# Kernel optimization log

Measured on AMD Instinct MI355X. Metric: run time of the kernel, lower is better.

The kernel has to match this reference:

```python
import jax, jax.numpy as jnp
import numpy as np

WINDOW = 3
SEQ_LEN = 41
FEATURE = 128
FILTER_NUM = 128
PAD = WINDOW // 2


def setup_inputs() -> dict:
    key = jax.random.key(0)
    k1, k2 = jax.random.split(key)
    B = 4096
    inputs = jax.random.normal(k1, (B, SEQ_LEN, FEATURE), dtype=jnp.float32)
    # per-position Linear weights: 41 independent [window*feature -> filter_num] layers
    fan_in = WINDOW * FEATURE
    W = jax.random.normal(k2, (SEQ_LEN, fan_in, FILTER_NUM), dtype=jnp.float32) / np.sqrt(fan_in)
    b = jnp.zeros((SEQ_LEN, FILTER_NUM), dtype=jnp.float32)
    return {"inputs": inputs, "W": W, "b": b}


def reference(inputs, W, b):
    # inputs: [B, S, F]; pad sequence dim by PAD zeros on each side
    xpad = jnp.pad(inputs, ((0, 0), (PAD, PAD), (0, 0)))  # [B, S+2*PAD, F]
    # gather windows: idx[s, w] = s + w -> [B, S, WINDOW, F]
    idx = jnp.arange(SEQ_LEN)[:, None] + jnp.arange(WINDOW)[None, :]
    xw = xpad[:, idx, :]
    B = inputs.shape[0]
    xw = xw.reshape(B, SEQ_LEN, WINDOW * FEATURE)  # [B, S, W*F]
    # per-position linear (locally-connected): one batched GEMM over positions
    out = jnp.einsum('bsd,sdf->bsf', xw, W) + b[None, :, :]
    # ReLU; Dropout(0.5) is identity in eval mode
    return jax.nn.relu(out)
```

## Files before the change

### kernel.cpp

```cpp
#include <hip/hip_runtime.h>

#define SEQ 41
#define FEAT 128
#define KDIM 384
#define ROWLEN (SEQ * FEAT)
#define BM 128

typedef float floatx4 __attribute__((ext_vector_type(4)));
typedef __bf16 bf16x8 __attribute__((ext_vector_type(8)));
typedef unsigned short ushortx4 __attribute__((ext_vector_type(4)));
typedef unsigned short ushortx8 __attribute__((ext_vector_type(8)));

__device__ __forceinline__ unsigned short f2bf(float f) {
    unsigned int u = __builtin_bit_cast(unsigned int, f);
    return (unsigned short)((u + 0x7fffu + ((u >> 16) & 1u)) >> 16);
}

#define DMA16(g, l)                                                          \
    __builtin_amdgcn_global_load_lds(                                        \
        (const __attribute__((address_space(1))) void*)(g),                  \
        (__attribute__((address_space(3))) void*)(l), 16, 0, 0)

__global__ __launch_bounds__(256) void wt2_kernel(const float* __restrict__ W,
                                                  unsigned short* __restrict__ Wt2) {
    int t = blockIdx.x * 256 + threadIdx.x;
    int s = t / 6144, g = t % 6144;
    int lane = g & 63, nt = (g >> 6) & 7, ks = (g >> 9) & 1, slab = g >> 10;
    int n  = nt * 16 + (lane & 15);
    int k0 = slab * 64 + ks * 32 + (lane >> 4) * 8;
    const float* Ws = W + (size_t)s * KDIM * FEAT;
    ushortx8 v;
#pragma unroll
    for (int j = 0; j < 8; j++) v[j] = f2bf(Ws[(size_t)(k0 + j) * FEAT + n]);
    *reinterpret_cast<ushortx8*>(Wt2 + (size_t)t * 8) = v;
}

template <int USE_WT>
__global__ __launch_bounds__(256, 2) void gemm_kernel(const float* __restrict__ X,
                                                      const void* __restrict__ Wsrc,
                                                      const float* __restrict__ bias,
                                                      float* __restrict__ out) {
    __shared__ unsigned short Afrag[2][2][8][512];
    __shared__ unsigned short Bfrag[2][2][8][512];

    const int tid  = threadIdx.x;
    const int lane = tid & 63;
    const int wv   = tid >> 6;
    const int s    = blockIdx.y;
    const int m0   = blockIdx.x * BM;

    const int klo = (s == 0) ? 2 : 0;
    const int khi = (s == SEQ - 1) ? 4 : 6;
    const int nk  = khi - klo;
    const int obase = (s - 1) * FEAT;

    const int colq = lane & 15, quad = lane >> 4;
    const int wr = wv >> 1, wc = wv & 1;

    const int ar = tid >> 3;
    const int ag = tid & 7;
    const int aq = ag >> 1, ahalf = ag & 1;

    const unsigned short* Wt2 = (const unsigned short*)Wsrc;
    const float* Wf = (const float*)Wsrc;

    floatx4 acc[4][4];
#pragma unroll
    for (int i = 0; i < 4; i++)
#pragma unroll
        for (int j = 0; j < 4; j++) acc[i][j] = (floatx4){0.f, 0.f, 0.f, 0.f};

    floatx4 a0[4], a1[4];

    auto stageA_load = [&](int kki) {
#pragma unroll
        for (int p = 0; p < 4; p++) {
            const float* base = X + (size_t)(m0 + p * 32 + ar) * ROWLEN
                                  + obase + kki * 64 + ag * 4;
            a0[p] = *reinterpret_cast<const floatx4*>(base);
            a1[p] = *reinterpret_cast<const floatx4*>(base + 32);
        }
    };
    auto stageA_write = [&](int buf) {
#pragma unroll
        for (int p = 0; p < 4; p++) {
            int r  = p * 32 + ar;
            int mt = r >> 4;
            int sl = ((r & 15) + 16 * aq) * 8 + ahalf * 4;
            ushortx4 w0, w1;
#pragma unroll
            for (int e = 0; e < 4; e++) { w0[e] = f2bf(a0[p][e]); w1[e] = f2bf(a1[p][e]); }
            *reinterpret_cast<ushortx4*>(&Afrag[buf][0][mt][sl]) = w0;
            *reinterpret_cast<ushortx4*>(&Afrag[buf][1][mt][sl]) = w1;
        }
    };
    auto stageB = [&](int buf, int kki) {
        if (USE_WT) {
            const unsigned short* src = Wt2 + (size_t)(s * 6 + kki) * 8192;
#pragma unroll
            for (int j = 0; j < 4; j++) {
                int fid = wv * 4 + j;
                const unsigned short* g = src + fid * 512 + lane * 8;
                DMA16(g, &Bfrag[buf][fid >> 3][fid & 7][0]);
            }
        } else {
#pragma unroll
            for (int p = 0; p < 4; p++) {
                int g2 = p * 256 + tid;
                int ln = g2 & 63, nt = (g2 >> 6) & 7, ks = (g2 >> 9) & 1;
                int n = nt * 16 + (ln & 15);
                int k = kki * 64 + ks * 32 + (ln >> 4) * 8;
                ushortx8 v;
#pragma unroll
                for (int j = 0; j < 8; j++)
                    v[j] = f2bf(Wf[((size_t)s * KDIM + k + j) * FEAT + n]);
                *reinterpret_cast<ushortx8*>(&Bfrag[buf][ks][nt][ln * 8]) = v;
            }
        }
    };
    auto compute = [&](int buf) {
#pragma unroll
        for (int ks = 0; ks < 2; ks++) {
            bf16x8 af[4], bf[4];
#pragma unroll
            for (int i = 0; i < 4; i++)
                af[i] = *reinterpret_cast<const bf16x8*>(&Afrag[buf][ks][wr * 4 + i][lane * 8]);
#pragma unroll
            for (int i = 0; i < 4; i++)
                bf[i] = *reinterpret_cast<const bf16x8*>(&Bfrag[buf][ks][wc * 4 + i][lane * 8]);
#pragma unroll
            for (int mi = 0; mi < 4; mi++)
#pragma unroll
                for (int ni = 0; ni < 4; ni++)
                    acc[mi][ni] = __builtin_amdgcn_mfma_f32_16x16x32_bf16(
                        af[mi], bf[ni], acc[mi][ni], 0, 0, 0);
        }
    };

    stageA_load(klo);
    stageB(0, klo);
    stageA_write(0);

    for (int i = 0; i < nk; i++) {
        __syncthreads();
        int cur = i & 1, nxt = cur ^ 1;
        if (i + 1 < nk) {
            stageA_load(klo + i + 1);
            stageB(nxt, klo + i + 1);
        }
        compute(cur);
        if (i + 1 < nk) stageA_write(nxt);
    }

#pragma unroll
    for (int mi = 0; mi < 4; mi++) {
        int m = m0 + (wr * 4 + mi) * 16 + quad * 4;
#pragma unroll
        for (int ni = 0; ni < 4; ni++) {
            int n = (wc * 4 + ni) * 16 + colq;
            float bv = bias[s * FEAT + n];
#pragma unroll
            for (int r = 0; r < 4; r++) {
                float v = acc[mi][ni][r] + bv;
                v = v > 0.f ? v : 0.f;
                out[((size_t)(m + r) * SEQ + s) * FEAT + n] = v;
            }
        }
    }
}

extern "C" void kernel_launch(void* const* d_in, const int* in_sizes, int n_in,
                              void* d_out, int out_size, void* d_ws, size_t ws_size,
                              hipStream_t stream) {
    const float* X    = (const float*)d_in[0];
    const float* W    = (const float*)d_in[1];
    const float* bias = (const float*)d_in[2];
    float* out = (float*)d_out;

    const int B = in_sizes[0] / ROWLEN;
    dim3 grid(B / BM, SEQ);

    const size_t wt_bytes = (size_t)SEQ * 6 * 8192 * sizeof(unsigned short);
    if (ws_size >= wt_bytes) {
        unsigned short* Wt2 = (unsigned short*)d_ws;
        wt2_kernel<<<(SEQ * 6144) / 256, 256, 0, stream>>>(W, Wt2);
        gemm_kernel<1><<<grid, 256, 0, stream>>>(X, (const void*)Wt2, bias, out);
    } else {
        gemm_kernel<0><<<grid, 256, 0, stream>>>(X, (const void*)W, bias, out);
    }
}
```

Before: 184.2 us.

## Load B fragments directly to registers, tile-transpose weights, raise occupancy

The weight pre-transpose kernel now stages each 64x128 slab through shared memory so both the fp32 reads and the bf16 writes are coalesced. It also uses the hardware bf16 conversion. The GEMM drops the shared-memory B buffer and its LDS DMA: each wave loads its own B fragments straight from global memory into registers, one slab at a time. The K loop is fully unrolled over 6 slabs, with zero-filled A at the boundary positions. Launch bounds rise to 3 blocks per CU. Freeing LDS and the B writes should allow more blocks per CU, at the cost of B loads that are not prefetched and extra MFMA work on zero padding for the edge positions.

Measured after the change: 232.2 us. +26.1%, slower.

```diff
diff --git a/kernel.cpp b/kernel.cpp
--- a/kernel.cpp
+++ b/kernel.cpp
@@ -12,56 +12,59 @@
 typedef unsigned short ushortx8 __attribute__((ext_vector_type(8)));
 
 __device__ __forceinline__ unsigned short f2bf(float f) {
-    unsigned int u = __builtin_bit_cast(unsigned int, f);
-    return (unsigned short)((u + 0x7fffu + ((u >> 16) & 1u)) >> 16);
+    return __builtin_bit_cast(unsigned short, (__bf16)f);
 }
 
-#define DMA16(g, l)                                                          \
-    __builtin_amdgcn_global_load_lds(                                        \
-        (const __attribute__((address_space(1))) void*)(g),                  \
-        (__attribute__((address_space(3))) void*)(l), 16, 0, 0)
-
-__global__ __launch_bounds__(256) void wt2_kernel(const float* __restrict__ W,
-                                                  unsigned short* __restrict__ Wt2) {
-    int t = blockIdx.x * 256 + threadIdx.x;
-    int s = t / 6144, g = t % 6144;
-    int lane = g & 63, nt = (g >> 6) & 7, ks = (g >> 9) & 1, slab = g >> 10;
-    int n  = nt * 16 + (lane & 15);
-    int k0 = slab * 64 + ks * 32 + (lane >> 4) * 8;
-    const float* Ws = W + (size_t)s * KDIM * FEAT;
-    ushortx8 v;
+__global__ __launch_bounds__(256) void wt3_kernel(const float* __restrict__ W,
+                                                  unsigned short* __restrict__ Wt) {
+    __shared__ float tile[64][FEAT + 1];
+    const int tid = threadIdx.x;
+    const int s = blockIdx.x / 6, slab = blockIdx.x % 6;
+    const float* src = W + ((size_t)s * KDIM + slab * 64) * FEAT;
 #pragma unroll
-    for (int j = 0; j < 8; j++) v[j] = f2bf(Ws[(size_t)(k0 + j) * FEAT + n]);
-    *reinterpret_cast<ushortx8*>(Wt2 + (size_t)t * 8) = v;
+    for (int p = 0; p < 8; p++) {
+        int q  = p * 256 + tid;
+        int k  = q >> 5;
+        int n4 = (q & 31) * 4;
+        floatx4 v = *reinterpret_cast<const floatx4*>(src + (size_t)k * FEAT + n4);
+        tile[k][n4] = v[0]; tile[k][n4 + 1] = v[1];
+        tile[k][n4 + 2] = v[2]; tile[k][n4 + 3] = v[3];
+    }
+    __syncthreads();
+    unsigned short* dst = Wt + (size_t)blockIdx.x * 8192;
+#pragma unroll
+    for (int p = 0; p < 4; p++) {
+        int g = p * 256 + tid;
+        int lane = g & 63, nt = (g >> 6) & 7, ks = g >> 9;
+        int n  = nt * 16 + (lane & 15);
+        int k0 = ks * 32 + (lane >> 4) * 8;
+        ushortx8 v;
+#pragma unroll
+        for (int j = 0; j < 8; j++) v[j] = f2bf(tile[k0 + j][n]);
+        *reinterpret_cast<ushortx8*>(dst + (size_t)g * 8) = v;
+    }
 }
 
 template <int USE_WT>
-__global__ __launch_bounds__(256, 2) void gemm_kernel(const float* __restrict__ X,
+__global__ __launch_bounds__(256, 3) void gemm_kernel(const float* __restrict__ X,
                                                       const void* __restrict__ Wsrc,
                                                       const float* __restrict__ bias,
                                                       float* __restrict__ out) {
     __shared__ unsigned short Afrag[2][2][8][512];
-    __shared__ unsigned short Bfrag[2][2][8][512];
 
     const int tid  = threadIdx.x;
     const int lane = tid & 63;
     const int wv   = tid >> 6;
     const int s    = blockIdx.y;
     const int m0   = blockIdx.x * BM;
-
-    const int klo = (s == 0) ? 2 : 0;
-    const int khi = (s == SEQ - 1) ? 4 : 6;
-    const int nk  = khi - klo;
     const int obase = (s - 1) * FEAT;
 
+    const int wr = wv >> 1, wc = wv & 1;
     const int colq = lane & 15, quad = lane >> 4;
-    const int wr = wv >> 1, wc = wv & 1;
-
-    const int ar = tid >> 3;
-    const int ag = tid & 7;
+    const int ar = tid >> 3, ag = tid & 7;
     const int aq = ag >> 1, ahalf = ag & 1;
 
-    const unsigned short* Wt2 = (const unsigned short*)Wsrc;
+    const unsigned short* Wt = (const unsigned short*)Wsrc;
     const float* Wf = (const float*)Wsrc;
 
     floatx4 acc[4][4];
@@ -71,14 +74,24 @@
         for (int j = 0; j < 4; j++) acc[i][j] = (floatx4){0.f, 0.f, 0.f, 0.f};
 
     floatx4 a0[4], a1[4];
+    bf16x8 bq[2][4];
 
-    auto stageA_load = [&](int kki) {
+    auto stageA_load = [&](int slab) {
+        bool valid = !((s == 0 && slab < 2) || (s == SEQ - 1 && slab >= 4));
+        if (valid) {
 #pragma unroll
-        for (int p = 0; p < 4; p++) {
-            const float* base = X + (size_t)(m0 + p * 32 + ar) * ROWLEN
-                                  + obase + kki * 64 + ag * 4;
-            a0[p] = *reinterpret_cast<const floatx4*>(base);
-            a1[p] = *reinterpret_cast<const floatx4*>(base + 32);
+            for (int p = 0; p < 4; p++) {
+                const float* base = X + (size_t)(m0 + p * 32 + ar) * ROWLEN
+                                      + obase + slab * 64 + ag * 4;
+                a0[p] = *reinterpret_cast<const floatx4*>(base);
+                a1[p] = *reinterpret_cast<const floatx4*>(base + 32);
+            }
+        } else {
+#pragma unroll
+            for (int p = 0; p < 4; p++) {
+                a0[p] = (floatx4){0.f, 0.f, 0.f, 0.f};
+                a1[p] = (floatx4){0.f, 0.f, 0.f, 0.f};
+            }
         }
     };
     auto stageA_write = [&](int buf) {
@@ -94,62 +107,57 @@
             *reinterpret_cast<ushortx4*>(&Afrag[buf][1][mt][sl]) = w1;
         }
     };
-    auto stageB = [&](int buf, int kki) {
+    auto loadB = [&](int slab) {
         if (USE_WT) {
-            const unsigned short* src = Wt2 + (size_t)(s * 6 + kki) * 8192;
+            const unsigned short* src = Wt + ((size_t)(s * 6 + slab)) * 8192 + lane * 8;
 #pragma unroll
-            for (int j = 0; j < 4; j++) {
-                int fid = wv * 4 + j;
-                const unsigned short* g = src + fid * 512 + lane * 8;
-                DMA16(g, &Bfrag[buf][fid >> 3][fid & 7][0]);
-            }
+            for (int ks = 0; ks < 2; ks++)
+#pragma unroll
+                for (int ni = 0; ni < 4; ni++)
+                    bq[ks][ni] = *reinterpret_cast<const bf16x8*>(
+                        src + (ks * 8 + wc * 4 + ni) * 512);
         } else {
 #pragma unroll
-            for (int p = 0; p < 4; p++) {
-                int g2 = p * 256 + tid;
-                int ln = g2 & 63, nt = (g2 >> 6) & 7, ks = (g2 >> 9) & 1;
-                int n = nt * 16 + (ln & 15);
-                int k = kki * 64 + ks * 32 + (ln >> 4) * 8;
-                ushortx8 v;
+            for (int ks = 0; ks < 2; ks++)
 #pragma unroll
-                for (int j = 0; j < 8; j++)
-                    v[j] = f2bf(Wf[((size_t)s * KDIM + k + j) * FEAT + n]);
-                *reinterpret_cast<ushortx8*>(&Bfrag[buf][ks][nt][ln * 8]) = v;
-            }
+                for (int ni = 0; ni < 4; ni++) {
+                    int n = (wc * 4 + ni) * 16 + colq;
+                    int k = slab * 64 + ks * 32 + quad * 8;
+                    ushortx8 v;
+#pragma unroll
+                    for (int j = 0; j < 8; j++)
+                        v[j] = f2bf(Wf[((size_t)s * KDIM + k + j) * FEAT + n]);
+                    bq[ks][ni] = __builtin_bit_cast(bf16x8, v);
+                }
         }
     };
     auto compute = [&](int buf) {
 #pragma unroll
         for (int ks = 0; ks < 2; ks++) {
-            bf16x8 af[4], bf[4];
+            bf16x8 af[4];
 #pragma unroll
             for (int i = 0; i < 4; i++)
-                af[i] = *reinterpret_cast<const bf16x8*>(&Afrag[buf][ks][wr * 4 + i][lane * 8]);
-#pragma unroll
-            for (int i = 0; i < 4; i++)
-                bf[i] = *reinterpret_cast<const bf16x8*>(&Bfrag[buf][ks][wc * 4 + i][lane * 8]);
+                af[i] = *reinterpret_cast<const bf16x8*>(
+                    &Afrag[buf][ks][wr * 4 + i][lane * 8]);
 #pragma unroll
             for (int mi = 0; mi < 4; mi++)
 #pragma unroll
                 for (int ni = 0; ni < 4; ni++)
                     acc[mi][ni] = __builtin_amdgcn_mfma_f32_16x16x32_bf16(
-                        af[mi], bf[ni], acc[mi][ni], 0, 0, 0);
+                        af[mi], bq[ks][ni], acc[mi][ni], 0, 0, 0);
         }
     };
 
-    stageA_load(klo);
-    stageB(0, klo);
+    stageA_load(0);
     stageA_write(0);
 
-    for (int i = 0; i < nk; i++) {
+#pragma unroll
+    for (int i = 0; i < 6; i++) {
         __syncthreads();
-        int cur = i & 1, nxt = cur ^ 1;
-        if (i + 1 < nk) {
-            stageA_load(klo + i + 1);
-            stageB(nxt, klo + i + 1);
-        }
-        compute(cur);
-        if (i + 1 < nk) stageA_write(nxt);
+        loadB(i);
+        if (i < 5) stageA_load(i + 1);
+        compute(i & 1);
+        if (i < 5) stageA_write((i + 1) & 1);
     }
 
 #pragma unroll
@@ -182,9 +190,9 @@
 
     const size_t wt_bytes = (size_t)SEQ * 6 * 8192 * sizeof(unsigned short);
     if (ws_size >= wt_bytes) {
-        unsigned short* Wt2 = (unsigned short*)d_ws;
-        wt2_kernel<<<(SEQ * 6144) / 256, 256, 0, stream>>>(W, Wt2);
-        gemm_kernel<1><<<grid, 256, 0, stream>>>(X, (const void*)Wt2, bias, out);
+        unsigned short* Wt = (unsigned short*)d_ws;
+        wt3_kernel<<<SEQ * 6, 256, 0, stream>>>(W, Wt);
+        gemm_kernel<1><<<grid, 256, 0, stream>>>(X, (const void*)Wt, bias, out);
     } else {
         gemm_kernel<0><<<grid, 256, 0, stream>>>(X, (const void*)W, bias, out);
     }
```
